# Performance work log

Measured on AMD Instinct MI355X. Metric: run time of the kernel, lower is better.

The kernel has to match this reference:

```python
import jax, jax.numpy as jnp
import numpy as np

EPS = 1e-5

@jax.custom_vjp
def spike(u):
    return (u >= 0).astype(u.dtype)

def _spike_fwd(u):
    return spike(u), u

def _spike_bwd(u, g):
    return (g / (1.0 + 5.0 * jnp.abs(u)) ** 2,)

spike.defvjp(_spike_fwd, _spike_bwd)


def setup_inputs() -> dict:
    key = jax.random.key(0)
    ks = jax.random.split(key, 20)
    B, T, IN, TH, H = 2048, 320, 64, 128, 64
    d = {}
    d['x'] = jax.random.normal(ks[0], (B, T, IN), jnp.float32)
    d['tda'] = jax.random.normal(ks[1], (B, 150), jnp.float32)
    # depthwise conv: Conv1d(64,128,k=15,pad=7,groups=64) -> kernel [128, 1, 15]
    d['conv_w'] = jax.random.normal(ks[2], (TH, 1, 15), jnp.float32) * 0.1
    d['conv_b'] = jnp.zeros((TH,), jnp.float32)
    d['bn1_g'] = jnp.ones((TH,), jnp.float32)
    d['bn1_b'] = jnp.zeros((TH,), jnp.float32)
    d['bn1_m'] = jnp.zeros((TH,), jnp.float32)
    d['bn1_v'] = jnp.ones((TH,), jnp.float32)
    # spatial_fc: Linear(128,64), init mean=0.05 std=0.1
    d['sp_w'] = 0.05 + 0.1 * jax.random.normal(ks[3], (H, TH), jnp.float32)
    d['sp_b'] = jnp.zeros((H,), jnp.float32)
    d['li_w'] = jax.random.normal(ks[4], (H, 2 * H), jnp.float32) * (1.0 / np.sqrt(2 * H))
    d['li_b'] = jnp.zeros((H,), jnp.float32)
    d['tda_w1'] = jax.random.normal(ks[5], (64, 150), jnp.float32) * (1.0 / np.sqrt(150))
    d['tda_b1'] = jnp.zeros((64,), jnp.float32)
    d['tda_w2'] = jax.random.normal(ks[6], (32, 64), jnp.float32) * 0.125
    d['tda_b2'] = jnp.zeros((32,), jnp.float32)
    dp_out = (320 // 32) * H  # 640
    d['cls_w1'] = jax.random.normal(ks[7], (128, dp_out + 32), jnp.float32) * (1.0 / np.sqrt(dp_out + 32))
    d['cls_b1'] = jnp.zeros((128,), jnp.float32)
    d['bn2_g'] = jnp.ones((128,), jnp.float32)
    d['bn2_b'] = jnp.zeros((128,), jnp.float32)
    d['bn2_m'] = jnp.zeros((128,), jnp.float32)
    d['bn2_v'] = jnp.ones((128,), jnp.float32)
    d['cls_w2'] = jax.random.normal(ks[8], (4, 128), jnp.float32) * (1.0 / np.sqrt(128))
    d['cls_b2'] = jnp.zeros((4,), jnp.float32)
    return d


def reference(x, tda, conv_w, conv_b, bn1_g, bn1_b, bn1_m, bn1_v, sp_w, sp_b,
              li_w, li_b, tda_w1, tda_b1, tda_w2, tda_b2,
              cls_w1, cls_b1, bn2_g, bn2_b, bn2_m, bn2_v, cls_w2, cls_b2):
    B, T, _ = x.shape
    L_DP, N_DP, H = 32, 16, 64
    # temp_conv (eval mode: no dropout, BN with running stats)
    xc = jnp.transpose(x, (0, 2, 1))  # [B, 64, T]
    y = jax.lax.conv_general_dilated(
        xc, conv_w, window_strides=(1,), padding=[(7, 7)],
        dimension_numbers=('NCH', 'OIH', 'NCH'), feature_group_count=64)
    y = y + conv_b[None, :, None]
    y = (y - bn1_m[None, :, None]) * jax.lax.rsqrt(bn1_v + EPS)[None, :, None] * bn1_g[None, :, None] + bn1_b[None, :, None]
    y = jax.nn.relu(y)
    y = jnp.transpose(y, (0, 2, 1))  # [B, T, 128]
    # precompute all input currents: [T, B, 64] (time-major for scan)
    cur_all = jnp.einsum('bth,oh->tbo', y, sp_w) + sp_b

    def step(carry, cur):
        mf, ms, ml = carry
        mf = 0.5 * mf + cur
        sf = spike(mf - 0.5)
        mf = mf * (1.0 - sf)
        ms = 0.9 * ms + cur
        ss = spike(ms - 1.0)
        ms = ms * (1.0 - ss)
        cur_li = jnp.concatenate([sf, ss], axis=-1) @ li_w.T + li_b
        ml = 0.9 * ml + cur_li
        return (mf, ms, ml), ml

    z0 = jnp.zeros((B, H), x.dtype)
    _, li_seq = jax.lax.scan(step, (z0, z0, z0), cur_all)  # [T, B, 64]
    li_seq = jnp.transpose(li_seq, (1, 0, 2))  # [B, T, 64]

    windows = li_seq.reshape(B, T // L_DP, L_DP, H)
    start_mean = windows[:, :, :N_DP, :].mean(axis=2)
    end_mean = windows[:, :, -N_DP:, :].mean(axis=2)
    dp_feat = (end_mean - start_mean).reshape(B, -1)  # [B, 640]

    t1 = jax.nn.relu(tda @ tda_w1.T + tda_b1)
    tda_feat = jax.nn.relu(t1 @ tda_w2.T + tda_b2)  # [B, 32]

    h = jnp.concatenate([dp_feat, tda_feat], axis=-1) @ cls_w1.T + cls_b1
    h = (h - bn2_m) * jax.lax.rsqrt(bn2_v + EPS) * bn2_g + bn2_b
    h = jax.nn.relu(h)
    return h @ cls_w2.T + cls_b2  # [B, 4]
```

## Files before the change

### kernel.cpp

```cpp
#include <hip/hip_runtime.h>

#define NT 256

#define WS_SPWT    0
#define WS_SC1     8192
#define WS_SH1     8320
#define WS_SC2     8448
#define WS_SH2     8576
#define WS_LIWT    8704
#define WS_TW1T    16896
#define WS_TW2T    26496
#define WS_CW1T    28544
#define WS_TOTAL   114560
#define WS_WG      114560
#define WS_WBASE   114688
#define WS_CURBASE (114688 + 2048*1280)
#define CUR_STRIDE 20480

__global__ void prep_kernel(
    const float* __restrict__ conv_b, const float* __restrict__ bn1_g,
    const float* __restrict__ bn1_b,  const float* __restrict__ bn1_m,
    const float* __restrict__ bn1_v,  const float* __restrict__ sp_w,
    const float* __restrict__ li_w,   const float* __restrict__ tda_w1,
    const float* __restrict__ tda_w2, const float* __restrict__ cls_w1,
    const float* __restrict__ bn2_g,  const float* __restrict__ bn2_b,
    const float* __restrict__ bn2_m,  const float* __restrict__ bn2_v,
    float* __restrict__ ws)
{
    int i = blockIdx.x * NT + threadIdx.x;
    if (i > WS_TOTAL) return;
    if (i == WS_TOTAL) {
        float g = 0.f, sE = 0.f, sL = 0.f; int w = 0;
        for (int t = 0; t < 320; ++t) {
            g = fmaf(0.9f, g, 1.f);
            int pos = t & 31;
            if (pos < 16) sE += g; else sL += g;
            if (pos == 31) { ws[WS_WG + w] = sL - sE; ++w; sE = 0.f; sL = 0.f; }
        }
        return;
    }
    if (i < WS_SC1) {
        int c = i >> 6, h = i & 63;
        ws[i] = sp_w[h*128 + c];
    } else if (i < WS_SH1) {
        int c = i - WS_SC1;
        float vv = bn1_v[c] + 1e-5f;
        ws[i] = (float)((double)bn1_g[c] / sqrt((double)vv));
    } else if (i < WS_SC2) {
        int c = i - WS_SH1;
        float vv = bn1_v[c] + 1e-5f;
        double s = (double)bn1_g[c] / sqrt((double)vv);
        ws[i] = (float)(((double)conv_b[c] - (double)bn1_m[c])*s + (double)bn1_b[c]);
    } else if (i < WS_SH2) {
        int c = i - WS_SC2;
        float vv = bn2_v[c] + 1e-5f;
        ws[i] = (float)((double)bn2_g[c] / sqrt((double)vv));
    } else if (i < WS_LIWT) {
        int c = i - WS_SH2;
        float vv = bn2_v[c] + 1e-5f;
        double s = (double)bn2_g[c] / sqrt((double)vv);
        ws[i] = (float)((double)bn2_b[c] - (double)bn2_m[c]*s);
    } else if (i < WS_TW1T) {
        int t = i - WS_LIWT; int j = t >> 6, o = t & 63;
        ws[i] = li_w[o*128 + j];
    } else if (i < WS_TW2T) {
        int t = i - WS_TW1T; int r = t >> 6, o = t & 63;
        ws[i] = tda_w1[o*150 + r];
    } else if (i < WS_CW1T) {
        int t = i - WS_TW2T; int j = t >> 5, o = t & 31;
        ws[i] = tda_w2[o*64 + j];
    } else {
        int t = i - WS_CW1T; int j = t >> 7, c = t & 127;
        ws[i] = cls_w1[c*672 + j];
    }
}

__launch_bounds__(NT, 4)
__global__ void convproj_kernel(
    const float* __restrict__ x, const float* __restrict__ conv_w,
    const float* __restrict__ ws, float* __restrict__ cur, int b0)
{
    __shared__ float y_lds[128*65];

    const int tid = threadIdx.x;
    const int bi  = blockIdx.x / 5;
    const int chk = blockIdx.x % 5;
    const int t0  = chk * 64;
    const int ic  = tid & 63;
    const int tg  = tid >> 6;

    float w0[15], w1[15];
    #pragma unroll
    for (int k = 0; k < 15; ++k) {
        w0[k] = conv_w[(2*ic)*15 + k];
        w1[k] = conv_w[(2*ic + 1)*15 + k];
    }
    const float sA = ws[WS_SC1 + 2*ic],     hA = ws[WS_SH1 + 2*ic];
    const float sB = ws[WS_SC1 + 2*ic + 1], hB = ws[WS_SH1 + 2*ic + 1];

    const float* xb = x + (size_t)(b0 + bi) * 20480 + ic;
    float xr[30];
    #pragma unroll
    for (int r = 0; r < 30; ++r) {
        int t = t0 + tg*16 - 7 + r;
        xr[r] = ((unsigned)t < 320u) ? xb[(size_t)t * 64] : 0.f;
    }

    #pragma unroll
    for (int j = 0; j < 16; ++j) {
        float a0 = 0.f, a1 = 0.f;
        #pragma unroll
        for (int k = 0; k < 15; ++k) {
            a0 = fmaf(xr[j + k], w0[k], a0);
            a1 = fmaf(xr[j + k], w1[k], a1);
        }
        int tt = tg*16 + j;
        y_lds[(2*ic)*65 + tt]     = fmaxf(fmaf(a0, sA, hA), 0.f);
        y_lds[(2*ic + 1)*65 + tt] = fmaxf(fmaf(a1, sB, hB), 0.f);
    }
    __syncthreads();

    {
        const int lane = tid & 63;
        const int h0 = __builtin_amdgcn_readfirstlane((tid >> 6) << 4);
        const float* __restrict__ spwT = ws;

        float acc[16];
        #pragma unroll
        for (int j = 0; j < 16; ++j) acc[j] = 0.f;
        #pragma unroll 4
        for (int c = 0; c < 128; ++c) {
            float yv = y_lds[c*65 + lane];
            const float4* wp = reinterpret_cast<const float4*>(spwT + c*64 + h0);
            float4 q0 = wp[0], q1 = wp[1], q2 = wp[2], q3 = wp[3];
            acc[0]  = fmaf(yv, q0.x, acc[0]);
            acc[1]  = fmaf(yv, q0.y, acc[1]);
            acc[2]  = fmaf(yv, q0.z, acc[2]);
            acc[3]  = fmaf(yv, q0.w, acc[3]);
            acc[4]  = fmaf(yv, q1.x, acc[4]);
            acc[5]  = fmaf(yv, q1.y, acc[5]);
            acc[6]  = fmaf(yv, q1.z, acc[6]);
            acc[7]  = fmaf(yv, q1.w, acc[7]);
            acc[8]  = fmaf(yv, q2.x, acc[8]);
            acc[9]  = fmaf(yv, q2.y, acc[9]);
            acc[10] = fmaf(yv, q2.z, acc[10]);
            acc[11] = fmaf(yv, q2.w, acc[11]);
            acc[12] = fmaf(yv, q3.x, acc[12]);
            acc[13] = fmaf(yv, q3.y, acc[13]);
            acc[14] = fmaf(yv, q3.z, acc[14]);
            acc[15] = fmaf(yv, q3.w, acc[15]);
        }
        float* cb = cur + (size_t)bi * CUR_STRIDE + (size_t)h0 * 320 + t0 + lane;
        #pragma unroll
        for (int j = 0; j < 16; ++j)
            cb[(size_t)j*320] = acc[j];
    }
}

__device__ __forceinline__ void lif16(float4 n0, float4 n1, float4 n2, float4 n3,
    float spb, float& mf, float& ms, float& rlo, float& rhi,
    float& slo, float& shi)
{
    float v[16] = {n0.x,n0.y,n0.z,n0.w, n1.x,n1.y,n1.z,n1.w,
                   n2.x,n2.y,n2.z,n2.w, n3.x,n3.y,n3.z,n3.w};
    slo = 0.f; shi = 0.f;
    #pragma unroll
    for (int q = 0; q < 16; ++q) {
        float c = v[q] + spb;
        mf = fmaf(0.5f, mf, c);
        bool sf = (mf - 0.5f) >= 0.f;
        ms = fmaf(0.9f, ms, c);
        bool ss = (ms - 1.0f) >= 0.f;
        mf = sf ? 0.f : mf;
        ms = ss ? 0.f : ms;
        rlo = fmaf(0.9f, rlo, sf ? 1.f : 0.f);
        rhi = fmaf(0.9f, rhi, ss ? 1.f : 0.f);
        slo += rlo; shi += rhi;
    }
}

__global__ void scan_kernel(const float* __restrict__ cur,
                            const float* __restrict__ sp_b,
                            float* __restrict__ W, int b0, int nb)
{
    const int wv = (int)((blockIdx.x * (unsigned)blockDim.x + threadIdx.x) >> 6);
    if (wv >= nb) return;
    const int lane = threadIdx.x & 63;
    const float* cb = cur + (size_t)wv * CUR_STRIDE + (size_t)lane * 320;
    const float spb = sp_b[lane];
    float* Wb = W + (size_t)(b0 + wv) * 1280;

    float mf = 0.f, ms = 0.f, rlo = 0.f, rhi = 0.f;

    float4 A0 = *reinterpret_cast<const float4*>(cb);
    float4 A1 = *reinterpret_cast<const float4*>(cb + 4);
    float4 A2 = *reinterpret_cast<const float4*>(cb + 8);
    float4 A3 = *reinterpret_cast<const float4*>(cb + 12);
    float4 B0 = *reinterpret_cast<const float4*>(cb + 16);
    float4 B1 = *reinterpret_cast<const float4*>(cb + 20);
    float4 B2 = *reinterpret_cast<const float4*>(cb + 24);
    float4 B3 = *reinterpret_cast<const float4*>(cb + 28);

    #pragma unroll 1
    for (int tb = 0; tb < 20; tb += 2) {
        float sE_lo, sE_hi, slo, shi;
        lif16(A0, A1, A2, A3, spb, mf, ms, rlo, rhi, sE_lo, sE_hi);
        if (tb + 2 < 20) {
            const float* p = cb + (tb + 2) * 16;
            A0 = *reinterpret_cast<const float4*>(p);
            A1 = *reinterpret_cast<const float4*>(p + 4);
            A2 = *reinterpret_cast<const float4*>(p + 8);
            A3 = *reinterpret_cast<const float4*>(p + 12);
        }
        lif16(B0, B1, B2, B3, spb, mf, ms, rlo, rhi, slo, shi);
        if (tb + 3 < 20) {
            const float* p = cb + (tb + 3) * 16;
            B0 = *reinterpret_cast<const float4*>(p);
            B1 = *reinterpret_cast<const float4*>(p + 4);
            B2 = *reinterpret_cast<const float4*>(p + 8);
            B3 = *reinterpret_cast<const float4*>(p + 12);
        }
        int wdx = tb >> 1;
        Wb[wdx*128 + lane]      = slo - sE_lo;
        Wb[wdx*128 + 64 + lane] = shi - sE_hi;
    }
}

__global__ void epilogue_kernel(
    const float* __restrict__ tda,    const float* __restrict__ li_b,
    const float* __restrict__ tda_b1, const float* __restrict__ tda_b2,
    const float* __restrict__ cls_b1, const float* __restrict__ cls_w2,
    const float* __restrict__ cls_b2, const float* __restrict__ ws,
    const float* __restrict__ W,      float* __restrict__ out)
{
    __shared__ float Wl[1280];
    __shared__ float t1[64], tf[32], dp[640], h1[128];
    const int b = blockIdx.x, tid = threadIdx.x;

    for (int i = tid; i < 1280; i += NT)
        Wl[i] = W[(size_t)b*1280 + i];
    __syncthreads();

    const float* __restrict__ liwT = ws + WS_LIWT;
    const float* __restrict__ tw1T = ws + WS_TW1T;
    const float* __restrict__ tw2T = ws + WS_TW2T;
    const float* __restrict__ cw1T = ws + WS_CW1T;
    const float* tdab = tda + b*150;

    if (tid < 64) {
        float acc = tda_b1[tid];
        for (int i2 = 0; i2 < 150; ++i2)
            acc = fmaf(tdab[i2], tw1T[i2*64 + tid], acc);
        t1[tid] = fmaxf(acc, 0.f);
    }
    __syncthreads();
    if (tid < 32) {
        float acc = tda_b2[tid];
        #pragma unroll 8
        for (int j = 0; j < 64; ++j)
            acc = fmaf(t1[j], tw2T[j*32 + tid], acc);
        tf[tid] = fmaxf(acc, 0.f);
    }
    {
        int o = tid & 63;
        for (int w = tid >> 6; w < 10; w += 4) {
            float acc = li_b[o] * ws[WS_WG + w];
            #pragma unroll 4
            for (int j = 0; j < 128; ++j)
                acc = fmaf(Wl[w*128 + j], liwT[j*64 + o], acc);
            dp[w*64 + o] = 0.0625f * acc;
        }
    }
    __syncthreads();
    if (tid < 128) {
        float acc = cls_b1[tid];
        for (int j = 0; j < 640; ++j)
            acc = fmaf(dp[j], cw1T[j*128 + tid], acc);
        #pragma unroll 4
        for (int j = 0; j < 32; ++j)
            acc = fmaf(tf[j], cw1T[(640 + j)*128 + tid], acc);
        float s2 = ws[WS_SC2 + tid], sh2 = ws[WS_SH2 + tid];
        h1[tid] = fmaxf(fmaf(acc, s2, sh2), 0.f);
    }
    __syncthreads();
    if (tid < 4) {
        float acc = cls_b2[tid];
        for (int c = 0; c < 128; ++c)
            acc = fmaf(h1[c], cls_w2[tid*128 + c], acc);
        out[b*4 + tid] = acc;
    }
}

extern "C" void kernel_launch(void* const* d_in, const int* in_sizes, int n_in,
                              void* d_out, int out_size, void* d_ws, size_t ws_size,
                              hipStream_t stream) {
    const float* x      = (const float*)d_in[0];
    const float* tda    = (const float*)d_in[1];
    const float* conv_w = (const float*)d_in[2];
    const float* conv_b = (const float*)d_in[3];
    const float* bn1_g  = (const float*)d_in[4];
    const float* bn1_b  = (const float*)d_in[5];
    const float* bn1_m  = (const float*)d_in[6];
    const float* bn1_v  = (const float*)d_in[7];
    const float* sp_w   = (const float*)d_in[8];
    const float* sp_b   = (const float*)d_in[9];
    const float* li_w   = (const float*)d_in[10];
    const float* li_b   = (const float*)d_in[11];
    const float* tda_w1 = (const float*)d_in[12];
    const float* tda_b1 = (const float*)d_in[13];
    const float* tda_w2 = (const float*)d_in[14];
    const float* tda_b2 = (const float*)d_in[15];
    const float* cls_w1 = (const float*)d_in[16];
    const float* cls_b1 = (const float*)d_in[17];
    const float* bn2_g  = (const float*)d_in[18];
    const float* bn2_b  = (const float*)d_in[19];
    const float* bn2_m  = (const float*)d_in[20];
    const float* bn2_v  = (const float*)d_in[21];
    const float* cls_w2 = (const float*)d_in[22];
    const float* cls_b2 = (const float*)d_in[23];
    float* ws  = (float*)d_ws;
    float* out = (float*)d_out;

    const int B = in_sizes[0] / (320 * 64);

    prep_kernel<<<(WS_TOTAL + 1 + NT - 1)/NT, NT, 0, stream>>>(
        conv_b, bn1_g, bn1_b, bn1_m, bn1_v, sp_w,
        li_w, tda_w1, tda_w2, cls_w1,
        bn2_g, bn2_b, bn2_m, bn2_v, ws);

    long cap = (long)(ws_size / 4) - (long)WS_CURBASE;
    int nbg = (int)(cap / CUR_STRIDE);
    if (nbg < 1) nbg = 1;
    if (nbg > B) nbg = B;

    for (int g0 = 0; g0 < B; g0 += nbg) {
        int nb = (B - g0 < nbg) ? (B - g0) : nbg;
        convproj_kernel<<<nb*5, NT, 0, stream>>>(
            x, conv_w, ws, ws + WS_CURBASE, g0);
        scan_kernel<<<(nb + 3)/4, NT, 0, stream>>>(
            ws + WS_CURBASE, sp_b, ws + WS_WBASE, g0, nb);
    }

    epilogue_kernel<<<B, NT, 0, stream>>>(
        tda, li_b, tda_b1, tda_b2, cls_b1, cls_w2, cls_b2,
        ws, ws + WS_WBASE, out);
}
```

Before: 282.6 us.

## Fold spatial bias into projection, pack LIF traces, batch epilogue four samples per block

New measurement: 308.7 us. 1.09x slower.

```diff
diff --git a/kernel.cpp b/kernel.cpp
--- a/kernel.cpp
+++ b/kernel.cpp
@@ -1,6 +1,8 @@
 #include <hip/hip_runtime.h>
 
 #define NT 256
+
+typedef __attribute__((ext_vector_type(2))) float f32x2;
 
 #define WS_SPWT    0
 #define WS_SC1     8192
@@ -78,7 +80,8 @@
 __launch_bounds__(NT, 4)
 __global__ void convproj_kernel(
     const float* __restrict__ x, const float* __restrict__ conv_w,
-    const float* __restrict__ ws, float* __restrict__ cur, int b0)
+    const float* __restrict__ sp_b, const float* __restrict__ ws,
+    float* __restrict__ cur, int b0)
 {
     __shared__ float y_lds[128*65];
 
@@ -99,11 +102,18 @@
     const float sB = ws[WS_SC1 + 2*ic + 1], hB = ws[WS_SH1 + 2*ic + 1];
 
     const float* xb = x + (size_t)(b0 + bi) * 20480 + ic;
+    const int tbase = t0 + tg*16 - 7;
     float xr[30];
-    #pragma unroll
-    for (int r = 0; r < 30; ++r) {
-        int t = t0 + tg*16 - 7 + r;
-        xr[r] = ((unsigned)t < 320u) ? xb[(size_t)t * 64] : 0.f;
+    if (tbase >= 0 && tbase + 29 < 320) {
+        #pragma unroll
+        for (int r = 0; r < 30; ++r)
+            xr[r] = xb[(size_t)(tbase + r) * 64];
+    } else {
+        #pragma unroll
+        for (int r = 0; r < 30; ++r) {
+            int t = tbase + r;
+            xr[r] = ((unsigned)t < 320u) ? xb[(size_t)t * 64] : 0.f;
+        }
     }
 
     #pragma unroll
@@ -126,8 +136,13 @@
         const float* __restrict__ spwT = ws;
 
         float acc[16];
-        #pragma unroll
-        for (int j = 0; j < 16; ++j) acc[j] = 0.f;
+        const float4* bp = reinterpret_cast<const float4*>(sp_b + h0);
+        float4 b0v = bp[0], b1v = bp[1], b2v = bp[2], b3v = bp[3];
+        acc[0]=b0v.x; acc[1]=b0v.y; acc[2]=b0v.z; acc[3]=b0v.w;
+        acc[4]=b1v.x; acc[5]=b1v.y; acc[6]=b1v.z; acc[7]=b1v.w;
+        acc[8]=b2v.x; acc[9]=b2v.y; acc[10]=b2v.z; acc[11]=b2v.w;
+        acc[12]=b3v.x; acc[13]=b3v.y; acc[14]=b3v.z; acc[15]=b3v.w;
+
         #pragma unroll 4
         for (int c = 0; c < 128; ++c) {
             float yv = y_lds[c*65 + lane];
@@ -158,39 +173,40 @@
 }
 
 __device__ __forceinline__ void lif16(float4 n0, float4 n1, float4 n2, float4 n3,
-    float spb, float& mf, float& ms, float& rlo, float& rhi,
-    float& slo, float& shi)
+    float& mf, float& ms, f32x2& r, f32x2 nine, f32x2& sum)
 {
     float v[16] = {n0.x,n0.y,n0.z,n0.w, n1.x,n1.y,n1.z,n1.w,
                    n2.x,n2.y,n2.z,n2.w, n3.x,n3.y,n3.z,n3.w};
-    slo = 0.f; shi = 0.f;
+    sum = f32x2{0.f, 0.f};
     #pragma unroll
     for (int q = 0; q < 16; ++q) {
-        float c = v[q] + spb;
+        float c = v[q];
         mf = fmaf(0.5f, mf, c);
-        bool sf = (mf - 0.5f) >= 0.f;
+        bool sf = mf >= 0.5f;
         ms = fmaf(0.9f, ms, c);
-        bool ss = (ms - 1.0f) >= 0.f;
+        bool ss = ms >= 1.0f;
         mf = sf ? 0.f : mf;
         ms = ss ? 0.f : ms;
-        rlo = fmaf(0.9f, rlo, sf ? 1.f : 0.f);
-        rhi = fmaf(0.9f, rhi, ss ? 1.f : 0.f);
-        slo += rlo; shi += rhi;
+        f32x2 spk;
+        spk.x = sf ? 1.f : 0.f;
+        spk.y = ss ? 1.f : 0.f;
+        asm("v_pk_fma_f32 %0, %1, %0, %2" : "+v"(r) : "v"(nine), "v"(spk));
+        asm("v_pk_add_f32 %0, %1, %0"     : "+v"(sum) : "v"(r));
     }
 }
 
 __global__ void scan_kernel(const float* __restrict__ cur,
-                            const float* __restrict__ sp_b,
                             float* __restrict__ W, int b0, int nb)
 {
     const int wv = (int)((blockIdx.x * (unsigned)blockDim.x + threadIdx.x) >> 6);
     if (wv >= nb) return;
     const int lane = threadIdx.x & 63;
     const float* cb = cur + (size_t)wv * CUR_STRIDE + (size_t)lane * 320;
-    const float spb = sp_b[lane];
     float* Wb = W + (size_t)(b0 + wv) * 1280;
 
-    float mf = 0.f, ms = 0.f, rlo = 0.f, rhi = 0.f;
+    float mf = 0.f, ms = 0.f;
+    f32x2 r = {0.f, 0.f};
+    const f32x2 nine = {0.9f, 0.9f};
 
     float4 A0 = *reinterpret_cast<const float4*>(cb);
     float4 A1 = *reinterpret_cast<const float4*>(cb + 4);
@@ -203,8 +219,8 @@
 
     #pragma unroll 1
     for (int tb = 0; tb < 20; tb += 2) {
-        float sE_lo, sE_hi, slo, shi;
-        lif16(A0, A1, A2, A3, spb, mf, ms, rlo, rhi, sE_lo, sE_hi);
+        f32x2 sumE, sumL;
+        lif16(A0, A1, A2, A3, mf, ms, r, nine, sumE);
         if (tb + 2 < 20) {
             const float* p = cb + (tb + 2) * 16;
             A0 = *reinterpret_cast<const float4*>(p);
@@ -212,7 +228,7 @@
             A2 = *reinterpret_cast<const float4*>(p + 8);
             A3 = *reinterpret_cast<const float4*>(p + 12);
         }
-        lif16(B0, B1, B2, B3, spb, mf, ms, rlo, rhi, slo, shi);
+        lif16(B0, B1, B2, B3, mf, ms, r, nine, sumL);
         if (tb + 3 < 20) {
             const float* p = cb + (tb + 3) * 16;
             B0 = *reinterpret_cast<const float4*>(p);
@@ -221,8 +237,8 @@
             B3 = *reinterpret_cast<const float4*>(p + 12);
         }
         int wdx = tb >> 1;
-        Wb[wdx*128 + lane]      = slo - sE_lo;
-        Wb[wdx*128 + 64 + lane] = shi - sE_hi;
+        Wb[wdx*128 + lane]      = sumL.x - sumE.x;
+        Wb[wdx*128 + 64 + lane] = sumL.y - sumE.y;
     }
 }
 
@@ -231,63 +247,84 @@
     const float* __restrict__ tda_b1, const float* __restrict__ tda_b2,
     const float* __restrict__ cls_b1, const float* __restrict__ cls_w2,
     const float* __restrict__ cls_b2, const float* __restrict__ ws,
-    const float* __restrict__ W,      float* __restrict__ out)
-{
-    __shared__ float Wl[1280];
-    __shared__ float t1[64], tf[32], dp[640], h1[128];
-    const int b = blockIdx.x, tid = threadIdx.x;
-
-    for (int i = tid; i < 1280; i += NT)
-        Wl[i] = W[(size_t)b*1280 + i];
+    const float* __restrict__ W,      float* __restrict__ out, int B)
+{
+    __shared__ float Wl[4*1280];
+    __shared__ float t1[4][64], tf[4][32], dp[4][640], h1[4][128];
+    const int b0b = blockIdx.x * 4, tid = threadIdx.x;
+    const int nvalid = (B - b0b < 4) ? (B - b0b) : 4;
+
+    for (int i = tid; i < nvalid*1280; i += NT)
+        Wl[i] = W[(size_t)b0b*1280 + i];
     __syncthreads();
 
     const float* __restrict__ liwT = ws + WS_LIWT;
     const float* __restrict__ tw1T = ws + WS_TW1T;
     const float* __restrict__ tw2T = ws + WS_TW2T;
     const float* __restrict__ cw1T = ws + WS_CW1T;
-    const float* tdab = tda + b*150;
-
-    if (tid < 64) {
-        float acc = tda_b1[tid];
-        for (int i2 = 0; i2 < 150; ++i2)
-            acc = fmaf(tdab[i2], tw1T[i2*64 + tid], acc);
-        t1[tid] = fmaxf(acc, 0.f);
-    }
-    __syncthreads();
-    if (tid < 32) {
-        float acc = tda_b2[tid];
-        #pragma unroll 8
-        for (int j = 0; j < 64; ++j)
-            acc = fmaf(t1[j], tw2T[j*32 + tid], acc);
-        tf[tid] = fmaxf(acc, 0.f);
-    }
+
     {
-        int o = tid & 63;
-        for (int w = tid >> 6; w < 10; w += 4) {
-            float acc = li_b[o] * ws[WS_WG + w];
-            #pragma unroll 4
-            for (int j = 0; j < 128; ++j)
-                acc = fmaf(Wl[w*128 + j], liwT[j*64 + o], acc);
-            dp[w*64 + o] = 0.0625f * acc;
+        int bb = tid >> 6, o = tid & 63;
+        if (bb < nvalid) {
+            const float* tdab = tda + (size_t)(b0b + bb)*150;
+            float acc = tda_b1[o];
+            for (int i2 = 0; i2 < 150; ++i2)
+                acc = fmaf(tdab[i2], tw1T[i2*64 + o], acc);
+            t1[bb][o] = fmaxf(acc, 0.f);
         }
     }
     __syncthreads();
     if (tid < 128) {
-        float acc = cls_b1[tid];
-        for (int j = 0; j < 640; ++j)
-            acc = fmaf(dp[j], cw1T[j*128 + tid], acc);
-        #pragma unroll 4
-        for (int j = 0; j < 32; ++j)
-            acc = fmaf(tf[j], cw1T[(640 + j)*128 + tid], acc);
-        float s2 = ws[WS_SC2 + tid], sh2 = ws[WS_SH2 + tid];
-        h1[tid] = fmaxf(fmaf(acc, s2, sh2), 0.f);
-    }
-    __syncthreads();
-    if (tid < 4) {
-        float acc = cls_b2[tid];
-        for (int c = 0; c < 128; ++c)
-            acc = fmaf(h1[c], cls_w2[tid*128 + c], acc);
-        out[b*4 + tid] = acc;
+        int bb = tid >> 5, o = tid & 31;
+        if (bb < nvalid) {
+            float acc = tda_b2[o];
+            #pragma unroll 8
+            for (int j = 0; j < 64; ++j)
+                acc = fmaf(t1[bb][j], tw2T[j*32 + o], acc);
+            tf[bb][o] = fmaxf(acc, 0.f);
+        }
+    }
+    {
+        int bb = tid >> 6, o = tid & 63;
+        if (bb < nvalid) {
+            float lb = li_b[o];
+            for (int w = 0; w < 10; ++w) {
+                float acc = lb * ws[WS_WG + w];
+                const float* Wr = &Wl[bb*1280 + w*128];
+                #pragma unroll 4
+                for (int j = 0; j < 128; ++j)
+                    acc = fmaf(Wr[j], liwT[j*64 + o], acc);
+                dp[bb][w*64 + o] = 0.0625f * acc;
+            }
+        }
+    }
+    __syncthreads();
+    {
+        #pragma unroll
+        for (int rep = 0; rep < 2; ++rep) {
+            int idx = rep*NT + tid;
+            int bb = idx >> 7, c = idx & 127;
+            if (bb < nvalid) {
+                float acc = cls_b1[c];
+                for (int j = 0; j < 640; ++j)
+                    acc = fmaf(dp[bb][j], cw1T[j*128 + c], acc);
+                #pragma unroll 4
+                for (int j = 0; j < 32; ++j)
+                    acc = fmaf(tf[bb][j], cw1T[(640 + j)*128 + c], acc);
+                float s2 = ws[WS_SC2 + c], sh2 = ws[WS_SH2 + c];
+                h1[bb][c] = fmaxf(fmaf(acc, s2, sh2), 0.f);
+            }
+        }
+    }
+    __syncthreads();
+    if (tid < 16) {
+        int bb = tid >> 2, o = tid & 3;
+        if (bb < nvalid) {
+            float acc = cls_b2[o];
+            for (int c = 0; c < 128; ++c)
+                acc = fmaf(h1[bb][c], cls_w2[o*128 + c], acc);
+            out[(size_t)(b0b + bb)*4 + o] = acc;
+        }
     }
 }
 
@@ -336,12 +373,12 @@
     for (int g0 = 0; g0 < B; g0 += nbg) {
         int nb = (B - g0 < nbg) ? (B - g0) : nbg;
         convproj_kernel<<<nb*5, NT, 0, stream>>>(
-            x, conv_w, ws, ws + WS_CURBASE, g0);
+            x, conv_w, sp_b, ws, ws + WS_CURBASE, g0);
         scan_kernel<<<(nb + 3)/4, NT, 0, stream>>>(
-            ws + WS_CURBASE, sp_b, ws + WS_WBASE, g0, nb);
-    }
-
-    epilogue_kernel<<<B, NT, 0, stream>>>(
+            ws + WS_CURBASE, ws + WS_WBASE, g0, nb);
+    }
+
+    epilogue_kernel<<<(B + 3)/4, NT, 0, stream>>>(
         tda, li_b, tda_b1, tda_b2, cls_b1, cls_w2, cls_b2,
-        ws, ws + WS_WBASE, out);
-}
+        ws, ws + WS_WBASE, out, B);
+}
```
